# Optimization experiments

Hardware: AMD Instinct MI355X
Metric: run time of the kernel (lower is better)

## Reference

```python
import jax, jax.numpy as jnp
import numpy as np

LATENT = 256
HIDDEN = 512
NODE_F = 128
MAX_NODES = 50
B = 128


def _mk_linear(key, fan_in, fan_out):
    kw, kb = jax.random.split(key)
    bound = 1.0 / np.sqrt(fan_in)
    W = jax.random.uniform(kw, (fan_in, fan_out), jnp.float32, -bound, bound)
    b = jax.random.uniform(kb, (fan_out,), jnp.float32, -bound, bound)
    return W, b


def setup_inputs() -> dict:
    key = jax.random.key(0)
    ks = jax.random.split(key, 7)
    z = jax.random.normal(ks[0], (B, LATENT), jnp.float32)
    # node decoder: latent -> hidden -> hidden -> max_nodes*node_features
    nw1, nb1 = _mk_linear(ks[1], LATENT, HIDDEN)
    nw2, nb2 = _mk_linear(ks[2], HIDDEN, HIDDEN)
    nw3, nb3 = _mk_linear(ks[3], HIDDEN, MAX_NODES * NODE_F)
    # edge decoder: latent + 2*node_features -> hidden -> hidden//2 -> 1
    ew1, eb1 = _mk_linear(ks[4], LATENT + 2 * NODE_F, HIDDEN)
    ew2, eb2 = _mk_linear(ks[5], HIDDEN, HIDDEN // 2)
    ew3, eb3 = _mk_linear(ks[6], HIDDEN // 2, 1)
    return {"z": z,
            "nw1": nw1, "nb1": nb1, "nw2": nw2, "nb2": nb2, "nw3": nw3, "nb3": nb3,
            "ew1": ew1, "eb1": eb1, "ew2": ew2, "eb2": eb2, "ew3": ew3, "eb3": eb3}


def reference(z, nw1, nb1, nw2, nb2, nw3, nb3, ew1, eb1, ew2, eb2, ew3, eb3):
    # ---- node decoder ----
    h = jax.nn.relu(z @ nw1 + nb1)
    h = jax.nn.relu(h @ nw2 + nb2)
    node_logits = h @ nw3 + nb3                      # [B, MAX_NODES*NODE_F]
    node_feats = node_logits.reshape(z.shape[0], MAX_NODES, NODE_F)
    node_probs = jax.nn.sigmoid(node_feats)

    # ---- edge decoder: vectorize the O(N^2) python loop over upper-tri pairs ----
    # jnp.triu_indices matches the torch loop order: i ascending, j ascending per i.
    ii, jj = jnp.triu_indices(MAX_NODES, k=1)        # [P] each, P = 1225
    ni = node_feats[:, ii, :]                        # [B, P, NODE_F]
    nj = node_feats[:, jj, :]                        # [B, P, NODE_F]
    zb = jnp.broadcast_to(z[:, None, :], (z.shape[0], ii.shape[0], z.shape[1]))
    edge_in = jnp.concatenate([zb, ni, nj], axis=-1)  # [B, P, LATENT+2*NODE_F]
    e = jax.nn.relu(edge_in @ ew1 + eb1)             # [B, P, HIDDEN]
    e = jax.nn.relu(e @ ew2 + eb2)                   # [B, P, HIDDEN//2]
    edge_probs = jax.nn.sigmoid(e @ ew3 + eb3)[..., 0]  # [B, P]
    return node_probs, edge_probs
```

## Files before the change

kernel.cpp:

```cpp
#include <hip/hip_runtime.h>
#include <math.h>

#define LATENT 256
#define HIDDEN 512
#define NODE_F 128
#define MAX_NODES 50
#define NPAIRS 1225
#define BATCH 128
#define NODE_OUT 6400
#define MTILE 64
#define TPB 5
#define EDGE_BLOCKS 512

typedef __attribute__((ext_vector_type(8))) short short8;
typedef __attribute__((ext_vector_type(4))) float float4v;

__device__ __forceinline__ float bf2f(ushort u) {
    union { unsigned int i; float f; } v; v.i = ((unsigned int)u) << 16; return v.f;
}
__device__ __forceinline__ ushort f2bf(float f) {
    union { unsigned int i; float f; } v; v.f = f;
    unsigned int r = v.i + 0x7fffu + ((v.i >> 16) & 1u);
    return (ushort)(r >> 16);
}
__device__ __forceinline__ float sigmoidf(float x) {
    return 1.0f / (1.0f + __expf(-x));
}

#define TR3_B0   0
#define PREP_B0  800
#define ZC_B0    1824
#define ND_B0    2080
#define PT_B0    2336
#define PREPK_NB 2341

__global__ __launch_bounds__(256) void k_prep_all(
    const float* __restrict__ nw3, ushort* __restrict__ nw3T,
    const float* __restrict__ ew1, const float* __restrict__ ew2,
    ushort* __restrict__ ew2T, ushort* __restrict__ wijT,
    const float* __restrict__ z, const float* __restrict__ eb1,
    float* __restrict__ Zc,
    const float* __restrict__ nw1, const float* __restrict__ nb1,
    const float* __restrict__ nw2, const float* __restrict__ nb2,
    ushort* __restrict__ h2b, int* __restrict__ ptab)
{
    __shared__ float smem[64 * 65];
    int b = blockIdx.x;
    int tid = threadIdx.x;

    if (b < PREP_B0) {
        int bb = b - TR3_B0;
        int k0 = (bb & 7) * 64;
        int n0 = (bb >> 3) * 64;
        int tx = tid & 63, ty = tid >> 6;
#pragma unroll
        for (int r = 0; r < 16; r++) {
            int row = r * 4 + ty;
            smem[row * 65 + tx] = nw3[(k0 + row) * NODE_OUT + n0 + tx];
        }
        __syncthreads();
#pragma unroll
        for (int c = 0; c < 16; c++) {
            int n = c * 4 + ty;
            nw3T[(size_t)(n0 + n) * HIDDEN + k0 + tx] = f2bf(smem[tx * 65 + n]);
        }
    } else if (b < ZC_B0) {
        int t = (b - PREP_B0) * 256 + tid;
        if (t < 256 * 512) {
            int n = t >> 9, k = t & 511;
            ew2T[t] = f2bf(ew2[k * 256 + n]);
        } else {
            int u = t - 256 * 512;
            int n = u >> 7, k = u & 127;
            float s = (n < 512) ? ew1[(256 + k) * 512 + n] : ew1[(384 + k) * 512 + (n - 512)];
            wijT[u] = f2bf(s);
        }
    } else if (b < ND_B0) {
        int b2 = b - ZC_B0;
        int r = b2 >> 1, o = (b2 & 1) * 256 + tid;
        float* zs = smem;
        zs[tid] = z[r * LATENT + tid];
        __syncthreads();
        float acc = 0.f;
#pragma unroll 8
        for (int k = 0; k < LATENT; k++) acc += zs[k] * ew1[k * HIDDEN + o];
        Zc[r * HIDDEN + o] = acc + eb1[o];
    } else if (b < PT_B0) {
        int b2 = b - ND_B0;
        int r = b2 >> 1, half = b2 & 1;
        float* zs = smem;
        float* hs = smem + 256;
        zs[tid] = z[r * LATENT + tid];
        __syncthreads();
        float a0 = 0.f, a1 = 0.f;
#pragma unroll 8
        for (int k = 0; k < LATENT; k++) {
            float zk = zs[k];
            a0 += zk * nw1[k * HIDDEN + tid];
            a1 += zk * nw1[k * HIDDEN + tid + 256];
        }
        hs[tid]       = fmaxf(a0 + nb1[tid], 0.f);
        hs[tid + 256] = fmaxf(a1 + nb1[tid + 256], 0.f);
        __syncthreads();
        int o = half * 256 + tid;
        float acc = 0.f;
#pragma unroll 8
        for (int k = 0; k < HIDDEN; k++) acc += hs[k] * nw2[k * HIDDEN + o];
        acc += nb2[o];
        h2b[r * HIDDEN + o] = f2bf(fmaxf(acc, 0.f));
    } else {
        int p = (b - PT_B0) * 256 + tid;
        if (p < NPAIRS) {
            int i = 0, off = 0;
            while (p - off >= MAX_NODES - 1 - i) { off += MAX_NODES - 1 - i; ++i; }
            int j = i + 1 + (p - off);
            ptab[p] = (i << 8) | j;
        }
    }
}

__global__ __launch_bounds__(256, 4) void k_node_out_mfma(
    const ushort* __restrict__ h2b, const ushort* __restrict__ nw3T,
    const float* __restrict__ nb3, float* __restrict__ node_probs,
    ushort* __restrict__ node_feats)
{
    int tid = threadIdx.x;
    int wave = tid >> 6, lane = tid & 63;
    int m16 = lane & 15, quad = lane >> 4;
    int n0 = (blockIdx.x >> 2) * 64;
    int m0 = (blockIdx.x & 3) * 32;
    int col = n0 + wave * 16 + m16;

    float4v acc[2];
    acc[0] = (float4v)(0.f); acc[1] = (float4v)(0.f);

    const ushort* bb = nw3T + (size_t)col * HIDDEN;
    const ushort* a0p = h2b + (m0 + m16) * HIDDEN;
    const ushort* a1p = h2b + (m0 + 16 + m16) * HIDDEN;
#pragma unroll
    for (int it = 0; it < 16; ++it) {
        int kk = it * 32 + quad * 8;
        short8 b = *(const short8*)(bb + kk);
        short8 a0 = *(const short8*)(a0p + kk);
        short8 a1 = *(const short8*)(a1p + kk);
        acc[0] = __builtin_amdgcn_mfma_f32_16x16x32_bf16(a0, b, acc[0], 0, 0, 0);
        acc[1] = __builtin_amdgcn_mfma_f32_16x16x32_bf16(a1, b, acc[1], 0, 0, 0);
    }
    float bias = nb3[col];
#pragma unroll
    for (int mt = 0; mt < 2; mt++)
#pragma unroll
        for (int t = 0; t < 4; t++) {
            int row = m0 + mt * 16 + quad * 4 + t;
            float v = acc[mt][t] + bias;
            node_probs[(size_t)row * NODE_OUT + col] = sigmoidf(v);
            node_feats[(size_t)row * NODE_OUT + col] = f2bf(v);
        }
}

__global__ __launch_bounds__(256, 4) void k_uv(
    const ushort* __restrict__ nf, const ushort* __restrict__ wijT,
    ushort* __restrict__ UV)
{
    int tid = threadIdx.x;
    int wave = tid >> 6, lane = tid & 63;
    int m16 = lane & 15, quad = lane >> 4;
    int bm = blockIdx.x >> 2, bn = blockIdx.x & 3;
    int base = bn * 256 + wave * 64;
    int r0 = bm * 64;

    float4v acc[4][4];
#pragma unroll
    for (int mt = 0; mt < 4; mt++)
#pragma unroll
        for (int nt = 0; nt < 4; nt++) acc[mt][nt] = (float4v)(0.f);

#pragma unroll
    for (int k0 = 0; k0 < NODE_F; k0 += 32) {
        int kk = k0 + quad * 8;
        short8 a0 = *(const short8*)(nf + (r0 + m16) * NODE_F + kk);
        short8 a1 = *(const short8*)(nf + (r0 + 16 + m16) * NODE_F + kk);
        short8 a2 = *(const short8*)(nf + (r0 + 32 + m16) * NODE_F + kk);
        short8 a3 = *(const short8*)(nf + (r0 + 48 + m16) * NODE_F + kk);
#pragma unroll
        for (int nt = 0; nt < 4; nt++) {
            int n = base + nt * 16 + m16;
            short8 b = *(const short8*)(wijT + n * NODE_F + kk);
            acc[0][nt] = __builtin_amdgcn_mfma_f32_16x16x32_bf16(a0, b, acc[0][nt], 0, 0, 0);
            acc[1][nt] = __builtin_amdgcn_mfma_f32_16x16x32_bf16(a1, b, acc[1][nt], 0, 0, 0);
            acc[2][nt] = __builtin_amdgcn_mfma_f32_16x16x32_bf16(a2, b, acc[2][nt], 0, 0, 0);
            acc[3][nt] = __builtin_amdgcn_mfma_f32_16x16x32_bf16(a3, b, acc[3][nt], 0, 0, 0);
        }
    }
#pragma unroll
    for (int nt = 0; nt < 4; nt++) {
        int colg = base + nt * 16 + m16;
#pragma unroll
        for (int mt = 0; mt < 4; mt++)
#pragma unroll
            for (int t = 0; t < 4; t++) {
                int rr = r0 + mt * 16 + quad * 4 + t;
                UV[(size_t)rr * 1024 + colg] = f2bf(acc[mt][nt][t]);
            }
    }
}

__global__ __launch_bounds__(512, 2) void k_edge7(
    const float* __restrict__ Zc, const ushort* __restrict__ UV,
    const ushort* __restrict__ ew2T, const float* __restrict__ ew3,
    const float* __restrict__ eb2, const float* __restrict__ eb3,
    const int* __restrict__ ptab, float* __restrict__ out_edges)
{
    __shared__ __align__(16) ushort h1[2][MTILE][HIDDEN + 8];
    __shared__ float part[MTILE][8];
    __shared__ int uo5[TPB][MTILE], vo5[TPB][MTILE];

    int tid  = threadIdx.x;
    int blk  = blockIdx.x;
    int b    = blk >> 2;
    int ti0  = (blk & 3) * TPB;

    if (tid < MTILE) {
#pragma unroll
        for (int t = 0; t < TPB; t++) {
            int p = (ti0 + t) * MTILE + tid;
            if (p >= NPAIRS) p = NPAIRS - 1;
            int ij = ptab[p];
            uo5[t][tid] = (b * MAX_NODES + (ij >> 8)) * 1024;
            vo5[t][tid] = (b * MAX_NODES + (ij & 255)) * 1024 + 512;
        }
    }

    int wave = tid >> 6, lane = tid & 63;
    int m16 = lane & 15, quad = lane >> 4;
    int c8 = lane * 8;
    int kk0 = quad * 8;

    float4v zA = *(const float4v*)(Zc + b * HIDDEN + c8);
    float4v zB = *(const float4v*)(Zc + b * HIDDEN + c8 + 4);

    const ushort* bb0 = ew2T + (wave * 32 + m16) * HIDDEN;
    const ushort* bb1 = ew2T + (wave * 32 + 16 + m16) * HIDDEN;
    short8 Breg[16][2];
#pragma unroll
    for (int kc = 0; kc < 16; kc++) {
        Breg[kc][0] = *(const short8*)(bb0 + kc * 32 + kk0);
        Breg[kc][1] = *(const short8*)(bb1 + kc * 32 + kk0);
    }
    float eb2v[2], ew3v[2];
    eb2v[0] = eb2[wave * 32 + m16];      eb2v[1] = eb2[wave * 32 + 16 + m16];
    ew3v[0] = ew3[wave * 32 + m16];      ew3v[1] = ew3[wave * 32 + 16 + m16];

    __syncthreads();

#pragma unroll
    for (int rr = 0; rr < 8; rr++) {
        int r = wave * 8 + rr;
        short8 u8 = *(const short8*)(UV + uo5[0][r] + c8);
        short8 v8 = *(const short8*)(UV + vo5[0][r] + c8);
        short8 hh;
#pragma unroll
        for (int e = 0; e < 8; e++) {
            float zz = (e < 4) ? zA[e] : zB[e - 4];
            hh[e] = (short)f2bf(fmaxf(zz + bf2f((ushort)u8[e]) + bf2f((ushort)v8[e]), 0.f));
        }
        *(short8*)&h1[0][r][c8] = hh;
    }
    __syncthreads();

    for (int t = 0; t < TPB; t++) {
        int cur = t & 1, nxt = cur ^ 1;
        bool hasNext = (t + 1 < TPB);

        float4v acc2[4][2];
#pragma unroll
        for (int mt = 0; mt < 4; mt++)
#pragma unroll
            for (int nt = 0; nt < 2; nt++) acc2[mt][nt] = (float4v)(0.f);

        short8 uu[4], vv[4];
        if (hasNext) {
#pragma unroll
            for (int rr = 0; rr < 4; rr++) {
                int r = wave * 8 + rr;
                uu[rr] = *(const short8*)(UV + uo5[t + 1][r] + c8);
                vv[rr] = *(const short8*)(UV + vo5[t + 1][r] + c8);
            }
        }
#pragma unroll
        for (int it = 0; it < 8; ++it) {
            int kk = it * 32 + kk0;
            short8 a0 = *(const short8*)&h1[cur][m16][kk];
            short8 a1 = *(const short8*)&h1[cur][16 + m16][kk];
            short8 a2 = *(const short8*)&h1[cur][32 + m16][kk];
            short8 a3 = *(const short8*)&h1[cur][48 + m16][kk];
            acc2[0][0] = __builtin_amdgcn_mfma_f32_16x16x32_bf16(a0, Breg[it][0], acc2[0][0], 0, 0, 0);
            acc2[1][0] = __builtin_amdgcn_mfma_f32_16x16x32_bf16(a1, Breg[it][0], acc2[1][0], 0, 0, 0);
            acc2[2][0] = __builtin_amdgcn_mfma_f32_16x16x32_bf16(a2, Breg[it][0], acc2[2][0], 0, 0, 0);
            acc2[3][0] = __builtin_amdgcn_mfma_f32_16x16x32_bf16(a3, Breg[it][0], acc2[3][0], 0, 0, 0);
            acc2[0][1] = __builtin_amdgcn_mfma_f32_16x16x32_bf16(a0, Breg[it][1], acc2[0][1], 0, 0, 0);
            acc2[1][1] = __builtin_amdgcn_mfma_f32_16x16x32_bf16(a1, Breg[it][1], acc2[1][1], 0, 0, 0);
            acc2[2][1] = __builtin_amdgcn_mfma_f32_16x16x32_bf16(a2, Breg[it][1], acc2[2][1], 0, 0, 0);
            acc2[3][1] = __builtin_amdgcn_mfma_f32_16x16x32_bf16(a3, Breg[it][1], acc2[3][1], 0, 0, 0);
        }
        if (hasNext) {
#pragma unroll
            for (int rr = 0; rr < 4; rr++) {
                int r = wave * 8 + rr;
                short8 hh;
#pragma unroll
                for (int e = 0; e < 8; e++) {
                    float zz = (e < 4) ? zA[e] : zB[e - 4];
                    hh[e] = (short)f2bf(fmaxf(zz + bf2f((ushort)uu[rr][e]) + bf2f((ushort)vv[rr][e]), 0.f));
                }
                *(short8*)&h1[nxt][r][c8] = hh;
            }
#pragma unroll
            for (int rr = 0; rr < 4; rr++) {
                int r = wave * 8 + 4 + rr;
                uu[rr] = *(const short8*)(UV + uo5[t + 1][r] + c8);
                vv[rr] = *(const short8*)(UV + vo5[t + 1][r] + c8);
            }
        }
#pragma unroll
        for (int it = 8; it < 16; ++it) {
            int kk = it * 32 + kk0;
            short8 a0 = *(const short8*)&h1[cur][m16][kk];
            short8 a1 = *(const short8*)&h1[cur][16 + m16][kk];
            short8 a2 = *(const short8*)&h1[cur][32 + m16][kk];
            short8 a3 = *(const short8*)&h1[cur][48 + m16][kk];
            acc2[0][0] = __builtin_amdgcn_mfma_f32_16x16x32_bf16(a0, Breg[it][0], acc2[0][0], 0, 0, 0);
            acc2[1][0] = __builtin_amdgcn_mfma_f32_16x16x32_bf16(a1, Breg[it][0], acc2[1][0], 0, 0, 0);
            acc2[2][0] = __builtin_amdgcn_mfma_f32_16x16x32_bf16(a2, Breg[it][0], acc2[2][0], 0, 0, 0);
            acc2[3][0] = __builtin_amdgcn_mfma_f32_16x16x32_bf16(a3, Breg[it][0], acc2[3][0], 0, 0, 0);
            acc2[0][1] = __builtin_amdgcn_mfma_f32_16x16x32_bf16(a0, Breg[it][1], acc2[0][1], 0, 0, 0);
            acc2[1][1] = __builtin_amdgcn_mfma_f32_16x16x32_bf16(a1, Breg[it][1], acc2[1][1], 0, 0, 0);
            acc2[2][1] = __builtin_amdgcn_mfma_f32_16x16x32_bf16(a2, Breg[it][1], acc2[2][1], 0, 0, 0);
            acc2[3][1] = __builtin_amdgcn_mfma_f32_16x16x32_bf16(a3, Breg[it][1], acc2[3][1], 0, 0, 0);
        }
        if (hasNext) {
#pragma unroll
            for (int rr = 0; rr < 4; rr++) {
                int r = wave * 8 + 4 + rr;
                short8 hh;
#pragma unroll
                for (int e = 0; e < 8; e++) {
                    float zz = (e < 4) ? zA[e] : zB[e - 4];
                    hh[e] = (short)f2bf(fmaxf(zz + bf2f((ushort)uu[rr][e]) + bf2f((ushort)vv[rr][e]), 0.f));
                }
                *(short8*)&h1[nxt][r][c8] = hh;
            }
        }

#pragma unroll
        for (int mt = 0; mt < 4; mt++)
#pragma unroll
            for (int tt = 0; tt < 4; tt++) {
                float s = 0.f;
#pragma unroll
                for (int nt = 0; nt < 2; nt++)
                    s += fmaxf(acc2[mt][nt][tt] + eb2v[nt], 0.f) * ew3v[nt];
                s += __shfl_xor(s, 1);
                s += __shfl_xor(s, 2);
                s += __shfl_xor(s, 4);
                s += __shfl_xor(s, 8);
                if (m16 == 0) part[mt * 16 + quad * 4 + tt][wave] = s;
            }
        __syncthreads();

        if (tid < MTILE) {
            int p = (ti0 + t) * MTILE + tid;
            if (p < NPAIRS) {
                float v = eb3[0];
#pragma unroll
                for (int w = 0; w < 8; w++) v += part[tid][w];
                out_edges[b * NPAIRS + p] = sigmoidf(v);
            }
        }
        __syncthreads();
    }
}

extern "C" void kernel_launch(void* const* d_in, const int* in_sizes, int n_in,
                              void* d_out, int out_size, void* d_ws, size_t ws_size,
                              hipStream_t stream) {
    const float* z   = (const float*)d_in[0];
    const float* nw1 = (const float*)d_in[1];
    const float* nb1 = (const float*)d_in[2];
    const float* nw2 = (const float*)d_in[3];
    const float* nb2 = (const float*)d_in[4];
    const float* nw3 = (const float*)d_in[5];
    const float* nb3 = (const float*)d_in[6];
    const float* ew1 = (const float*)d_in[7];
    const float* eb1 = (const float*)d_in[8];
    const float* ew2 = (const float*)d_in[9];
    const float* eb2 = (const float*)d_in[10];
    const float* ew3 = (const float*)d_in[11];
    const float* eb3 = (const float*)d_in[12];

    char* ws = (char*)d_ws;
    int*    ptab = (int*)(ws);
    ushort* h2b  = (ushort*)(ws + 262144);
    ushort* nf   = (ushort*)(ws + 393216);
    ushort* ew2T = (ushort*)(ws + 2031616);
    ushort* wijT = (ushort*)(ws + 2293760);
    ushort* nw3T = (ushort*)(ws + 2555904);
    float*  Zc   = (float*)(ws + 9109504);
    ushort* UV   = (ushort*)(ws + 9371648);

    float* out_nodes = (float*)d_out;
    float* out_edges = out_nodes + BATCH * NODE_OUT;

    k_prep_all<<<PREPK_NB, 256, 0, stream>>>(nw3, nw3T, ew1, ew2, ew2T, wijT,
                                             z, eb1, Zc, nw1, nb1, nw2, nb2,
                                             h2b, ptab);
    k_node_out_mfma<<<400, 256, 0, stream>>>(h2b, nw3T, nb3, out_nodes, nf);
    k_uv<<<400, 256, 0, stream>>>(nf, wijT, UV);
    k_edge7<<<EDGE_BLOCKS, 512, 0, stream>>>(Zc, UV, ew2T, ew3,
                                             eb2, eb3, ptab, out_edges);
}
```

Before: 232.4 us.

## Enlarge edge and node-output tiles per block; use packed bf16 conversion

```diff
diff --git a/kernel.cpp b/kernel.cpp
--- a/kernel.cpp
+++ b/kernel.cpp
@@ -1,4 +1,5 @@
 #include <hip/hip_runtime.h>
+#include <hip/hip_bf16.h>
 #include <math.h>
 
 #define LATENT 256
@@ -9,11 +10,13 @@
 #define BATCH 128
 #define NODE_OUT 6400
 #define MTILE 64
-#define TPB 5
-#define EDGE_BLOCKS 512
+#define TPB 10
+#define EDGE_BLOCKS 256
 
 typedef __attribute__((ext_vector_type(8))) short short8;
 typedef __attribute__((ext_vector_type(4))) float float4v;
+
+union S8U { short8 s; unsigned int u[4]; };
 
 __device__ __forceinline__ float bf2f(ushort u) {
     union { unsigned int i; float f; } v; v.i = ((unsigned int)u) << 16; return v.f;
@@ -22,6 +25,10 @@
     union { unsigned int i; float f; } v; v.f = f;
     unsigned int r = v.i + 0x7fffu + ((v.i >> 16) & 1u);
     return (ushort)(r >> 16);
+}
+__device__ __forceinline__ unsigned int pk_bf16(float f0, float f1) {
+    __hip_bfloat162 p = __float22bfloat162_rn(float2{f0, f1});
+    unsigned int w; __builtin_memcpy(&w, &p, 4); return w;
 }
 __device__ __forceinline__ float sigmoidf(float x) {
     return 1.0f / (1.0f + __expf(-x));
@@ -127,28 +134,28 @@
     int tid = threadIdx.x;
     int wave = tid >> 6, lane = tid & 63;
     int m16 = lane & 15, quad = lane >> 4;
-    int n0 = (blockIdx.x >> 2) * 64;
-    int m0 = (blockIdx.x & 3) * 32;
+    int n0 = (blockIdx.x >> 1) * 64;
+    int m0 = (blockIdx.x & 1) * 64;
     int col = n0 + wave * 16 + m16;
 
-    float4v acc[2];
-    acc[0] = (float4v)(0.f); acc[1] = (float4v)(0.f);
+    float4v acc[4];
+#pragma unroll
+    for (int mt = 0; mt < 4; mt++) acc[mt] = (float4v)(0.f);
 
     const ushort* bb = nw3T + (size_t)col * HIDDEN;
-    const ushort* a0p = h2b + (m0 + m16) * HIDDEN;
-    const ushort* a1p = h2b + (m0 + 16 + m16) * HIDDEN;
 #pragma unroll
     for (int it = 0; it < 16; ++it) {
         int kk = it * 32 + quad * 8;
         short8 b = *(const short8*)(bb + kk);
-        short8 a0 = *(const short8*)(a0p + kk);
-        short8 a1 = *(const short8*)(a1p + kk);
-        acc[0] = __builtin_amdgcn_mfma_f32_16x16x32_bf16(a0, b, acc[0], 0, 0, 0);
-        acc[1] = __builtin_amdgcn_mfma_f32_16x16x32_bf16(a1, b, acc[1], 0, 0, 0);
+#pragma unroll
+        for (int mt = 0; mt < 4; mt++) {
+            short8 a = *(const short8*)(h2b + (m0 + mt * 16 + m16) * HIDDEN + kk);
+            acc[mt] = __builtin_amdgcn_mfma_f32_16x16x32_bf16(a, b, acc[mt], 0, 0, 0);
+        }
     }
     float bias = nb3[col];
 #pragma unroll
-    for (int mt = 0; mt < 2; mt++)
+    for (int mt = 0; mt < 4; mt++)
 #pragma unroll
         for (int t = 0; t < 4; t++) {
             int row = m0 + mt * 16 + quad * 4 + t;
@@ -205,7 +212,7 @@
     }
 }
 
-__global__ __launch_bounds__(512, 2) void k_edge7(
+__global__ __launch_bounds__(512, 2) void k_edge8(
     const float* __restrict__ Zc, const ushort* __restrict__ UV,
     const ushort* __restrict__ ew2T, const float* __restrict__ ew3,
     const float* __restrict__ eb2, const float* __restrict__ eb3,
@@ -217,8 +224,8 @@
 
     int tid  = threadIdx.x;
     int blk  = blockIdx.x;
-    int b    = blk >> 2;
-    int ti0  = (blk & 3) * TPB;
+    int b    = blk >> 1;
+    int ti0  = (blk & 1) * TPB;
 
     if (tid < MTILE) {
 #pragma unroll
@@ -258,13 +265,16 @@
         int r = wave * 8 + rr;
         short8 u8 = *(const short8*)(UV + uo5[0][r] + c8);
         short8 v8 = *(const short8*)(UV + vo5[0][r] + c8);
-        short8 hh;
-#pragma unroll
-        for (int e = 0; e < 8; e++) {
-            float zz = (e < 4) ? zA[e] : zB[e - 4];
-            hh[e] = (short)f2bf(fmaxf(zz + bf2f((ushort)u8[e]) + bf2f((ushort)v8[e]), 0.f));
-        }
-        *(short8*)&h1[0][r][c8] = hh;
+        S8U hh;
+#pragma unroll
+        for (int e2 = 0; e2 < 4; e2++) {
+            float z0 = (e2 < 2) ? zA[e2 * 2] : zB[e2 * 2 - 4];
+            float z1 = (e2 < 2) ? zA[e2 * 2 + 1] : zB[e2 * 2 - 3];
+            float f0 = fmaxf(z0 + bf2f((ushort)u8[e2 * 2]) + bf2f((ushort)v8[e2 * 2]), 0.f);
+            float f1 = fmaxf(z1 + bf2f((ushort)u8[e2 * 2 + 1]) + bf2f((ushort)v8[e2 * 2 + 1]), 0.f);
+            hh.u[e2] = pk_bf16(f0, f1);
+        }
+        *(short8*)&h1[0][r][c8] = hh.s;
     }
     __syncthreads();
 
@@ -307,13 +317,16 @@
 #pragma unroll
             for (int rr = 0; rr < 4; rr++) {
                 int r = wave * 8 + rr;
-                short8 hh;
-#pragma unroll
-                for (int e = 0; e < 8; e++) {
-                    float zz = (e < 4) ? zA[e] : zB[e - 4];
-                    hh[e] = (short)f2bf(fmaxf(zz + bf2f((ushort)uu[rr][e]) + bf2f((ushort)vv[rr][e]), 0.f));
+                S8U hh;
+#pragma unroll
+                for (int e2 = 0; e2 < 4; e2++) {
+                    float z0 = (e2 < 2) ? zA[e2 * 2] : zB[e2 * 2 - 4];
+                    float z1 = (e2 < 2) ? zA[e2 * 2 + 1] : zB[e2 * 2 - 3];
+                    float f0 = fmaxf(z0 + bf2f((ushort)uu[rr][e2 * 2]) + bf2f((ushort)vv[rr][e2 * 2]), 0.f);
+                    float f1 = fmaxf(z1 + bf2f((ushort)uu[rr][e2 * 2 + 1]) + bf2f((ushort)vv[rr][e2 * 2 + 1]), 0.f);
+                    hh.u[e2] = pk_bf16(f0, f1);
                 }
-                *(short8*)&h1[nxt][r][c8] = hh;
+                *(short8*)&h1[nxt][r][c8] = hh.s;
             }
 #pragma unroll
             for (int rr = 0; rr < 4; rr++) {
@@ -342,13 +355,16 @@
 #pragma unroll
             for (int rr = 0; rr < 4; rr++) {
                 int r = wave * 8 + 4 + rr;
-                short8 hh;
-#pragma unroll
-                for (int e = 0; e < 8; e++) {
-                    float zz = (e < 4) ? zA[e] : zB[e - 4];
-                    hh[e] = (short)f2bf(fmaxf(zz + bf2f((ushort)uu[rr][e]) + bf2f((ushort)vv[rr][e]), 0.f));
+                S8U hh;
+#pragma unroll
+                for (int e2 = 0; e2 < 4; e2++) {
+                    float z0 = (e2 < 2) ? zA[e2 * 2] : zB[e2 * 2 - 4];
+                    float z1 = (e2 < 2) ? zA[e2 * 2 + 1] : zB[e2 * 2 - 3];
+                    float f0 = fmaxf(z0 + bf2f((ushort)uu[rr][e2 * 2]) + bf2f((ushort)vv[rr][e2 * 2]), 0.f);
+                    float f1 = fmaxf(z1 + bf2f((ushort)uu[rr][e2 * 2 + 1]) + bf2f((ushort)vv[rr][e2 * 2 + 1]), 0.f);
+                    hh.u[e2] = pk_bf16(f0, f1);
                 }
-                *(short8*)&h1[nxt][r][c8] = hh;
+                *(short8*)&h1[nxt][r][c8] = hh.s;
             }
         }
 
@@ -414,8 +430,8 @@
     k_prep_all<<<PREPK_NB, 256, 0, stream>>>(nw3, nw3T, ew1, ew2, ew2T, wijT,
                                              z, eb1, Zc, nw1, nb1, nw2, nb2,
                                              h2b, ptab);
-    k_node_out_mfma<<<400, 256, 0, stream>>>(h2b, nw3T, nb3, out_nodes, nf);
+    k_node_out_mfma<<<200, 256, 0, stream>>>(h2b, nw3T, nb3, out_nodes, nf);
     k_uv<<<400, 256, 0, stream>>>(nf, wijT, UV);
-    k_edge7<<<EDGE_BLOCKS, 512, 0, stream>>>(Zc, UV, ew2T, ew3,
+    k_edge8<<<EDGE_BLOCKS, 512, 0, stream>>>(Zc, UV, ew2T, ew3,
                                              eb2, eb3, ptab, out_edges);
 }
```

Result: faster. 225.8 us (-2.9%).
